# Optimization experiments

Hardware: AMD Instinct MI355X
Metric: run time of the kernel (lower is better)

Reference implementation:

```python
import jax, jax.numpy as jnp
import numpy as np

CAT_SIZES = [31360, 6807, 18, 94]
TOTAL = int(sum(CAT_SIZES))          # 38279
EMB = 128
N_FIELDS = len(CAT_SIZES)
D_IN = N_FIELDS * EMB                # 512 (num_features is empty)
MLP_DIMS = [2048, 1024, 512]
B = 16384
OFFSETS = np.concatenate([[0], np.cumsum(CAT_SIZES)[:-1]]).astype(np.int32)


def setup_inputs() -> dict:
    key = jax.random.key(0)
    ks = jax.random.split(key, 20)
    # x holds raw per-field category ids stored as float32 (as the torch model expects)
    cols = [jax.random.randint(ks[i], (B,), 0, s) for i, s in enumerate(CAT_SIZES)]
    x = jnp.stack(cols, axis=1).astype(jnp.float32)

    bias = jnp.zeros((1,), jnp.float32)
    fc = jax.random.uniform(ks[4], (TOTAL, 1), dtype=jnp.float32)          # nn.Parameter(torch.rand)
    emb_table = jax.random.normal(ks[5], (TOTAL, EMB), dtype=jnp.float32)  # nn.Embedding default N(0,1)

    dims = [D_IN] + MLP_DIMS + [1]
    params = {}
    for i in range(len(dims) - 1):
        fan_in = dims[i]
        bound = 1.0 / np.sqrt(fan_in)
        params[f"W{i+1}"] = jax.random.uniform(ks[6 + 2 * i], (dims[i], dims[i + 1]), jnp.float32, -bound, bound)
        params[f"b{i+1}"] = jax.random.uniform(ks[7 + 2 * i], (dims[i + 1],), jnp.float32, -bound, bound)

    return dict(x=x, bias=bias, fc=fc, emb_table=emb_table, **params)


def reference(x, bias, fc, emb_table, W1, b1, W2, b2, W3, b3, W4, b4):
    cat = x.astype(jnp.int32)                       # [B, F] raw per-field ids
    b = cat.shape[0]

    # embedding lookup with RAW (un-offset) ids, faithful to the original code
    embed_x = emb_table[cat].reshape(b, -1)          # [B, F*EMB]

    # one_hot(offset ids) @ fc  ==  sum_f fc[offset ids]  (offset ranges disjoint)
    gidx = cat + jnp.asarray(OFFSETS)                # [B, F] global ids
    lin = jnp.sum(fc[gidx, 0], axis=1)               # [B]
    fm_y = bias + lin                                # [B]

    # FM term: embed_x is 2-D, so sum over dim=1 collapses features;
    # the keepdim sum over dim=-1 then collapses the BATCH dim to shape (1,)
    # (a quirk of the original code that we reproduce exactly)
    square_of_sum = jnp.sum(embed_x, axis=1) ** 2    # [B]
    sum_of_square = jnp.sum(embed_x ** 2, axis=1)    # [B]
    fm_y = fm_y + 0.5 * jnp.sum(square_of_sum - sum_of_square, axis=-1, keepdims=True)  # [B]
    fm_y = fm_y[:, None]                             # [B,1]

    # MLP (eval mode: dropout is identity)
    h = embed_x
    for W, bb in ((W1, b1), (W2, b2), (W3, b3)):
        h = jax.nn.relu(h @ W + bb)
    mlp_y = h @ W4 + b4                              # [B,1]

    return jax.nn.sigmoid(fm_y + mlp_y)              # [B,1]
```

## Files before the change

kernel.cpp:

```cpp
#include <hip/hip_runtime.h>
#include <hip/hip_fp8.h>
#include <cstdint>


typedef float f32x4 __attribute__((ext_vector_type(4)));
typedef int i32x4 __attribute__((ext_vector_type(4)));
typedef int i32x8 __attribute__((ext_vector_type(8)));

#define GLOAD16(gptr, lptr)                                                \
  __builtin_amdgcn_global_load_lds(                                        \
      (const __attribute__((address_space(1))) void*)(gptr),               \
      (__attribute__((address_space(3))) void*)(lptr), 16, 0, 0)

__device__ inline uint32_t f2fp4(float v) {
  uint32_t s = (__float_as_uint(v) >> 31) << 3;
  float a = fabsf(v);
  uint32_t m;
  if (a < 0.25f) m = 0;
  else if (a < 0.75f) m = 1;
  else if (a < 1.25f) m = 2;
  else if (a < 1.75f) m = 3;
  else if (a < 2.5f)  m = 4;
  else if (a < 3.5f)  m = 5;
  else if (a < 5.0f)  m = 6;
  else m = 7;
  return s | m;
}

static constexpr size_t OFF_LIN  = 0;
static constexpr size_t OFF_PART = 65536;
static constexpr size_t OFF_S    = 81920;
static constexpr size_t OFF_ACC  = 98304;
static constexpr size_t OFF_EMB  = 262144;
static constexpr size_t OFF_H1   = OFF_EMB + 8388608ull;
static constexpr size_t OFF_H2   = OFF_H1 + 33554432ull;
static constexpr size_t OFF_W1T  = OFF_H2 + 16777216ull;
static constexpr size_t OFF_W2T  = OFF_W1T + 524288ull;
static constexpr size_t OFF_W3T  = OFF_W2T + 1048576ull;

__global__ void prep(const float* __restrict__ W1, const float* __restrict__ W2,
                     const float* __restrict__ W3, uint8_t* __restrict__ W1T,
                     uint8_t* __restrict__ W2T, uint8_t* __restrict__ W3T,
                     const float* __restrict__ x, const float* __restrict__ fc,
                     const float* __restrict__ emb, uint8_t* __restrict__ ebf,
                     float* __restrict__ lin, float* __restrict__ partials) {
  __shared__ __align__(16) float smem[32 * 33];
  int blk = blockIdx.x;
  int tid = threadIdx.x;
  if (blk < 3584) {
    const float* W;
    uint8_t* WT;
    int K, N, bx, by;
    if (blk < 1024) {
      W = W1; WT = W1T; K = 512; N = 2048; bx = blk & 63; by = blk >> 6;
    } else if (blk < 3072) {
      int t = blk - 1024;
      W = W2; WT = W2T; K = 2048; N = 1024; bx = t & 31; by = t >> 5;
    } else {
      int t = blk - 3072;
      W = W3; WT = W3T; K = 1024; N = 512; bx = t & 15; by = t >> 4;
    }
    int tx = tid & 31, ty = tid >> 5;
    int n0 = bx * 32, k0 = by * 32;
#pragma unroll
    for (int i = ty; i < 32; i += 8)
      smem[i * 33 + tx] = W[(size_t)(k0 + i) * N + n0 + tx];
    __syncthreads();
    if (tx < 16) {
#pragma unroll
      for (int i = ty; i < 32; i += 8) {
        uint32_t lo = f2fp4(smem[(2 * tx) * 33 + i] * 128.f);
        uint32_t hi = f2fp4(smem[(2 * tx + 1) * 33 + i] * 128.f);
        WT[(size_t)(n0 + i) * (K >> 1) + (k0 >> 1) + tx] =
            (uint8_t)(lo | (hi << 4));
      }
    }
  } else {
    int gb = blk - 3584;
    int wv = tid >> 6, lane = tid & 63;
    int b = gb * 4 + wv;
    int f = lane >> 4;
    int idx = (int)x[b * 4 + f];
    const float* row = emb + (size_t)idx * 128 + (lane & 15) * 8;
    float4 v0 = ((const float4*)row)[0];
    float4 v1 = ((const float4*)row)[1];
    float s = v0.x + v0.y + v0.z + v0.w + v1.x + v1.y + v1.z + v1.w;
    float q = v0.x * v0.x + v0.y * v0.y + v0.z * v0.z + v0.w * v0.w +
              v1.x * v1.x + v1.y * v1.y + v1.z * v1.z + v1.w * v1.w;

    int lo = 0, hi = 0;
    lo = __builtin_amdgcn_cvt_pk_fp8_f32(v0.x, v0.y, lo, false);
    lo = __builtin_amdgcn_cvt_pk_fp8_f32(v0.z, v0.w, lo, true);
    hi = __builtin_amdgcn_cvt_pk_fp8_f32(v1.x, v1.y, hi, false);
    hi = __builtin_amdgcn_cvt_pk_fp8_f32(v1.z, v1.w, hi, true);
    int2 pk = make_int2(lo, hi);
    *(int2*)(ebf + (size_t)b * 512 + lane * 8) = pk;

    float lp = 0.f;
    if ((lane & 15) == 0) {
      int off = (f == 1) ? 31360 : (f == 2) ? 38167 : (f == 3) ? 38185 : 0;
      lp = fc[idx + off];
    }
#pragma unroll
    for (int m = 32; m; m >>= 1) {
      s += __shfl_xor(s, m);
      q += __shfl_xor(q, m);
      lp += __shfl_xor(lp, m);
    }
    float* pt = smem;
    if (lane == 0) {
      lin[b] = lp;
      pt[wv] = s * s - q;
    }
    __syncthreads();
    if (tid == 0) partials[gb] = pt[0] + pt[1] + pt[2] + pt[3];
  }
}

__global__ void reduce_partials(const float* __restrict__ p,
                                float* __restrict__ S,
                                float* __restrict__ dotacc) {
  int tid = threadIdx.x;
  float v = 0.f;
  for (int i = tid; i < 4096; i += 256) v += p[i];
#pragma unroll
  for (int m = 32; m; m >>= 1) v += __shfl_xor(v, m);
  __shared__ float ps[4];
  if ((tid & 63) == 0) ps[tid >> 6] = v;
  __syncthreads();
  if (tid == 0) S[0] = ps[0] + ps[1] + ps[2] + ps[3];
  float4 z4 = make_float4(0.f, 0.f, 0.f, 0.f);
  for (int i = tid; i < 4096; i += 256) ((float4*)dotacc)[i] = z4;
}

__global__ __launch_bounds__(256) void gemm_mx_relu(
    const uint8_t* __restrict__ A, const uint8_t* __restrict__ BT,
    const float* __restrict__ bias, uint8_t* __restrict__ C, int K, int N,
    int GX) {
  __shared__ __align__(16) uint8_t As[128][256];
  __shared__ __align__(16) uint8_t Bs[128][128];
  int bid = blockIdx.x;
  int by = (bid & 7) + ((bid >> 3) / GX) * 8;
  int bx = (bid >> 3) & (GX - 1);
  int tid = threadIdx.x;
  int wv = tid >> 6, lane = tid & 63;
  int m0 = by * 128, n0 = bx * 128;
  int mw = (wv >> 1) * 64, nw = (wv & 1) * 64;
  int ml = lane & 15, kg = lane >> 4;
  int Kb2 = K >> 1;
  int arow = lane >> 4;
  int brow = lane >> 3;
  int bcol = ((lane & 7) ^ brow) * 16;

  f32x4 acc[4][4];
#pragma unroll
  for (int i = 0; i < 4; ++i)
#pragma unroll
    for (int j = 0; j < 4; ++j) acc[i][j] = (f32x4){0.f, 0.f, 0.f, 0.f};

  for (int kt = 0; kt < K; kt += 256) {
#pragma unroll
    for (int r = 0; r < 8; ++r) {
      int g = r * 4 + wv;
      int trow = 4 * g + arow;
      int acol = ((lane & 15) ^ (trow & 15)) * 16;
      const uint8_t* ga = A + (size_t)(m0 + trow) * K + kt + acol;
      GLOAD16(ga, &As[4 * g][0]);
    }
#pragma unroll
    for (int r = 0; r < 4; ++r) {
      int g = r * 4 + wv;
      const uint8_t* gb =
          BT + (size_t)(n0 + 8 * g + brow) * Kb2 + (kt >> 1) + bcol;
      GLOAD16(gb, &Bs[8 * g][0]);
    }
    __syncthreads();

    i32x4 z = (i32x4){0, 0, 0, 0};
#pragma unroll
    for (int j = 0; j < 2; ++j) {
      int c0 = 8 * j + 2 * kg;
      int pa0 = (c0 ^ ml) * 16;
      int pa1 = ((c0 + 1) ^ ml) * 16;
      int pb = ((4 * j + kg) ^ (ml & 7)) * 16;
      i32x8 af[4], bfr[4];
#pragma unroll
      for (int t = 0; t < 4; ++t) {
        int ra = mw + t * 16 + ml;
        i32x4 a0 = *(const i32x4*)&As[ra][pa0];
        i32x4 a1 = *(const i32x4*)&As[ra][pa1];
        af[t] = __builtin_shufflevector(a0, a1, 0, 1, 2, 3, 4, 5, 6, 7);
        i32x4 vb = *(const i32x4*)&Bs[nw + t * 16 + ml][pb];
        bfr[t] = __builtin_shufflevector(vb, z, 0, 1, 2, 3, 4, 5, 6, 7);
      }
#pragma unroll
      for (int mt = 0; mt < 4; ++mt)
#pragma unroll
        for (int nt = 0; nt < 4; ++nt)
          acc[mt][nt] = __builtin_amdgcn_mfma_scale_f32_16x16x128_f8f6f4(
              af[mt], bfr[nt], acc[mt][nt],
               0,  4,
              0, 0x7F7F7F7F, 0, 0x78787878);
    }
    __syncthreads();
  }

  int rbase = kg * 4;
#pragma unroll
  for (int nt = 0; nt < 4; ++nt) {
    int col = n0 + nw + nt * 16 + ml;
    float bv = bias[col];
#pragma unroll
    for (int mt = 0; mt < 4; ++mt) {
      int row = m0 + mw + mt * 16 + rbase;
      float v0 = acc[mt][nt][0] + bv, v1 = acc[mt][nt][1] + bv;
      float v2 = acc[mt][nt][2] + bv, v3 = acc[mt][nt][3] + bv;
      v0 = v0 > 0.f ? v0 : 0.f;
      v1 = v1 > 0.f ? v1 : 0.f;
      v2 = v2 > 0.f ? v2 : 0.f;
      v3 = v3 > 0.f ? v3 : 0.f;
      int w01 = __builtin_amdgcn_cvt_pk_fp8_f32(v0, v1, 0, false);
      int w23 = __builtin_amdgcn_cvt_pk_fp8_f32(v2, v3, 0, false);
      C[(size_t)(row + 0) * N + col] = (uint8_t)(w01 & 0xFF);
      C[(size_t)(row + 1) * N + col] = (uint8_t)((w01 >> 8) & 0xFF);
      C[(size_t)(row + 2) * N + col] = (uint8_t)(w23 & 0xFF);
      C[(size_t)(row + 3) * N + col] = (uint8_t)((w23 >> 8) & 0xFF);
    }
  }
}

__global__ __launch_bounds__(256) void gemm_mx_dot(
    const uint8_t* __restrict__ A, const uint8_t* __restrict__ BT,
    const float* __restrict__ bias, const float* __restrict__ W4,
    float* __restrict__ dotacc, int K, int N, int GX) {
  __shared__ __align__(16) uint8_t As[128][256];
  __shared__ __align__(16) uint8_t Bs[128][128];
  int bid = blockIdx.x;
  int by = (bid & 7) + ((bid >> 3) / GX) * 8;
  int bx = (bid >> 3) & (GX - 1);
  int tid = threadIdx.x;
  int wv = tid >> 6, lane = tid & 63;
  int m0 = by * 128, n0 = bx * 128;
  int mw = (wv >> 1) * 64, nw = (wv & 1) * 64;
  int ml = lane & 15, kg = lane >> 4;
  int Kb2 = K >> 1;
  int arow = lane >> 4;
  int brow = lane >> 3;
  int bcol = ((lane & 7) ^ brow) * 16;

  f32x4 acc[4][4];
#pragma unroll
  for (int i = 0; i < 4; ++i)
#pragma unroll
    for (int j = 0; j < 4; ++j) acc[i][j] = (f32x4){0.f, 0.f, 0.f, 0.f};

  for (int kt = 0; kt < K; kt += 256) {
#pragma unroll
    for (int r = 0; r < 8; ++r) {
      int g = r * 4 + wv;
      int trow = 4 * g + arow;
      int acol = ((lane & 15) ^ (trow & 15)) * 16;
      const uint8_t* ga = A + (size_t)(m0 + trow) * K + kt + acol;
      GLOAD16(ga, &As[4 * g][0]);
    }
#pragma unroll
    for (int r = 0; r < 4; ++r) {
      int g = r * 4 + wv;
      const uint8_t* gb =
          BT + (size_t)(n0 + 8 * g + brow) * Kb2 + (kt >> 1) + bcol;
      GLOAD16(gb, &Bs[8 * g][0]);
    }
    __syncthreads();

    i32x4 z = (i32x4){0, 0, 0, 0};
#pragma unroll
    for (int j = 0; j < 2; ++j) {
      int c0 = 8 * j + 2 * kg;
      int pa0 = (c0 ^ ml) * 16;
      int pa1 = ((c0 + 1) ^ ml) * 16;
      int pb = ((4 * j + kg) ^ (ml & 7)) * 16;
      i32x8 af[4], bfr[4];
#pragma unroll
      for (int t = 0; t < 4; ++t) {
        int ra = mw + t * 16 + ml;
        i32x4 a0 = *(const i32x4*)&As[ra][pa0];
        i32x4 a1 = *(const i32x4*)&As[ra][pa1];
        af[t] = __builtin_shufflevector(a0, a1, 0, 1, 2, 3, 4, 5, 6, 7);
        i32x4 vb = *(const i32x4*)&Bs[nw + t * 16 + ml][pb];
        bfr[t] = __builtin_shufflevector(vb, z, 0, 1, 2, 3, 4, 5, 6, 7);
      }
#pragma unroll
      for (int mt = 0; mt < 4; ++mt)
#pragma unroll
        for (int nt = 0; nt < 4; ++nt)
          acc[mt][nt] = __builtin_amdgcn_mfma_scale_f32_16x16x128_f8f6f4(
              af[mt], bfr[nt], acc[mt][nt],
              0, 4, 0, 0x7F7F7F7F, 0, 0x78787878);
    }
    __syncthreads();
  }

  float bv[4], w4v[4];
#pragma unroll
  for (int nt = 0; nt < 4; ++nt) {
    int col = n0 + nw + nt * 16 + ml;
    bv[nt] = bias[col];
    w4v[nt] = W4[col];
  }
  int rbase = kg * 4;
#pragma unroll
  for (int mt = 0; mt < 4; ++mt) {
#pragma unroll
    for (int r = 0; r < 4; ++r) {
      float p = 0.f;
#pragma unroll
      for (int nt = 0; nt < 4; ++nt) {
        float v = acc[mt][nt][r] + bv[nt];
        v = v > 0.f ? v : 0.f;
        p += v * w4v[nt];
      }
#pragma unroll
      for (int m = 1; m < 16; m <<= 1) p += __shfl_xor(p, m);
      if (ml == 0)
        atomicAdd(&dotacc[m0 + mw + mt * 16 + rbase + r], p);
    }
  }
}

__global__ void final_out(const float* __restrict__ dotacc,
                          const float* __restrict__ lin,
                          const float* __restrict__ S,
                          const float* __restrict__ bias,
                          const float* __restrict__ b4,
                          float* __restrict__ out) {
  int i = blockIdx.x * 256 + threadIdx.x;
  float z = dotacc[i] + b4[0] + bias[0] + lin[i] + 0.5f * S[0];
  out[i] = 1.f / (1.f + expf(-z));
}

extern "C" void kernel_launch(void* const* d_in, const int* in_sizes, int n_in,
                              void* d_out, int out_size, void* d_ws,
                              size_t ws_size, hipStream_t stream) {
  const float* x    = (const float*)d_in[0];
  const float* bias = (const float*)d_in[1];
  const float* fc   = (const float*)d_in[2];
  const float* emb  = (const float*)d_in[3];
  const float* W1   = (const float*)d_in[4];
  const float* b1   = (const float*)d_in[5];
  const float* W2   = (const float*)d_in[6];
  const float* b2   = (const float*)d_in[7];
  const float* W3   = (const float*)d_in[8];
  const float* b3   = (const float*)d_in[9];
  const float* W4   = (const float*)d_in[10];
  const float* b4   = (const float*)d_in[11];
  float* out = (float*)d_out;

  char* ws = (char*)d_ws;
  float* lin    = (float*)(ws + OFF_LIN);
  float* part   = (float*)(ws + OFF_PART);
  float* Sp     = (float*)(ws + OFF_S);
  float* dacc   = (float*)(ws + OFF_ACC);
  uint8_t* EMBb = (uint8_t*)(ws + OFF_EMB);
  uint8_t* H1   = (uint8_t*)(ws + OFF_H1);
  uint8_t* H2   = (uint8_t*)(ws + OFF_H2);
  uint8_t* W1T  = (uint8_t*)(ws + OFF_W1T);
  uint8_t* W2T  = (uint8_t*)(ws + OFF_W2T);
  uint8_t* W3T  = (uint8_t*)(ws + OFF_W3T);

  prep<<<7680, 256, 0, stream>>>(W1, W2, W3, W1T, W2T, W3T, x, fc, emb, EMBb,
                                 lin, part);
  reduce_partials<<<1, 256, 0, stream>>>(part, Sp, dacc);

  gemm_mx_relu<<<2048, 256, 0, stream>>>(EMBb, W1T, b1, H1, 512, 2048, 16);
  gemm_mx_relu<<<1024, 256, 0, stream>>>(H1, W2T, b2, H2, 2048, 1024, 8);
  gemm_mx_dot<<<512, 256, 0, stream>>>(H2, W3T, b3, W4, dacc, 1024, 512, 4);

  final_out<<<64, 256, 0, stream>>>(dacc, lin, Sp, bias, b4, out);
}
```

Measured before the change: 174.8 us.

## Halve GEMM K-tile to 128 and fold partial reduction into other kernels

Removes the single-block reduce_partials launch. Zeroing of the dot accumulator moves into 16 extra prep blocks, and the FM partial sum is recomputed redundantly by every final_out block. The GEMM kernels now stage a 128-wide K tile instead of 256, which halves LDS use per block and changes the swizzle and load layout. This may allow more blocks per CU, at the cost of twice as many K iterations and barriers.

```diff
diff --git a/kernel.cpp b/kernel.cpp
--- a/kernel.cpp
+++ b/kernel.cpp
@@ -29,7 +29,6 @@
 
 static constexpr size_t OFF_LIN  = 0;
 static constexpr size_t OFF_PART = 65536;
-static constexpr size_t OFF_S    = 81920;
 static constexpr size_t OFF_ACC  = 98304;
 static constexpr size_t OFF_EMB  = 262144;
 static constexpr size_t OFF_H1   = OFF_EMB + 8388608ull;
@@ -43,7 +42,8 @@
                      uint8_t* __restrict__ W2T, uint8_t* __restrict__ W3T,
                      const float* __restrict__ x, const float* __restrict__ fc,
                      const float* __restrict__ emb, uint8_t* __restrict__ ebf,
-                     float* __restrict__ lin, float* __restrict__ partials) {
+                     float* __restrict__ lin, float* __restrict__ partials,
+                     float* __restrict__ dotacc) {
   __shared__ __align__(16) float smem[32 * 33];
   int blk = blockIdx.x;
   int tid = threadIdx.x;
@@ -75,7 +75,7 @@
             (uint8_t)(lo | (hi << 4));
       }
     }
-  } else {
+  } else if (blk < 7680) {
     int gb = blk - 3584;
     int wv = tid >> 6, lane = tid & 63;
     int b = gb * 4 + wv;
@@ -114,31 +114,18 @@
     }
     __syncthreads();
     if (tid == 0) partials[gb] = pt[0] + pt[1] + pt[2] + pt[3];
-  }
-}
-
-__global__ void reduce_partials(const float* __restrict__ p,
-                                float* __restrict__ S,
-                                float* __restrict__ dotacc) {
-  int tid = threadIdx.x;
-  float v = 0.f;
-  for (int i = tid; i < 4096; i += 256) v += p[i];
-#pragma unroll
-  for (int m = 32; m; m >>= 1) v += __shfl_xor(v, m);
-  __shared__ float ps[4];
-  if ((tid & 63) == 0) ps[tid >> 6] = v;
-  __syncthreads();
-  if (tid == 0) S[0] = ps[0] + ps[1] + ps[2] + ps[3];
-  float4 z4 = make_float4(0.f, 0.f, 0.f, 0.f);
-  for (int i = tid; i < 4096; i += 256) ((float4*)dotacc)[i] = z4;
+  } else {
+    int zb = blk - 7680;
+    ((float4*)dotacc)[zb * 256 + tid] = make_float4(0.f, 0.f, 0.f, 0.f);
+  }
 }
 
 __global__ __launch_bounds__(256) void gemm_mx_relu(
     const uint8_t* __restrict__ A, const uint8_t* __restrict__ BT,
     const float* __restrict__ bias, uint8_t* __restrict__ C, int K, int N,
     int GX) {
-  __shared__ __align__(16) uint8_t As[128][256];
-  __shared__ __align__(16) uint8_t Bs[128][128];
+  __shared__ __align__(16) uint8_t As[128][128];
+  __shared__ __align__(16) uint8_t Bs[128][64];
   int bid = blockIdx.x;
   int by = (bid & 7) + ((bid >> 3) / GX) * 8;
   int bx = (bid >> 3) & (GX - 1);
@@ -148,9 +135,13 @@
   int mw = (wv >> 1) * 64, nw = (wv & 1) * 64;
   int ml = lane & 15, kg = lane >> 4;
   int Kb2 = K >> 1;
-  int arow = lane >> 4;
-  int brow = lane >> 3;
-  int bcol = ((lane & 7) ^ brow) * 16;
+  int asrow = lane >> 3;
+  int ascol = ((lane & 7) ^ asrow) * 16;
+  int bsrow = lane >> 2;
+  int bscol = ((lane & 3) ^ (bsrow & 3)) * 16;
+  int pa0 = ((2 * kg) ^ (ml & 7)) * 16;
+  int pa1 = ((2 * kg + 1) ^ (ml & 7)) * 16;
+  int pb = (kg ^ (ml & 3)) * 16;
 
   f32x4 acc[4][4];
 #pragma unroll
@@ -158,50 +149,41 @@
 #pragma unroll
     for (int j = 0; j < 4; ++j) acc[i][j] = (f32x4){0.f, 0.f, 0.f, 0.f};
 
-  for (int kt = 0; kt < K; kt += 256) {
-#pragma unroll
-    for (int r = 0; r < 8; ++r) {
-      int g = r * 4 + wv;
-      int trow = 4 * g + arow;
-      int acol = ((lane & 15) ^ (trow & 15)) * 16;
-      const uint8_t* ga = A + (size_t)(m0 + trow) * K + kt + acol;
-      GLOAD16(ga, &As[4 * g][0]);
-    }
+  for (int kt = 0; kt < K; kt += 128) {
 #pragma unroll
     for (int r = 0; r < 4; ++r) {
       int g = r * 4 + wv;
+      const uint8_t* ga = A + (size_t)(m0 + 8 * g + asrow) * K + kt + ascol;
+      GLOAD16(ga, &As[8 * g][0]);
+    }
+#pragma unroll
+    for (int r = 0; r < 2; ++r) {
+      int g = r * 4 + wv;
       const uint8_t* gb =
-          BT + (size_t)(n0 + 8 * g + brow) * Kb2 + (kt >> 1) + bcol;
-      GLOAD16(gb, &Bs[8 * g][0]);
+          BT + (size_t)(n0 + 16 * g + bsrow) * Kb2 + (kt >> 1) + bscol;
+      GLOAD16(gb, &Bs[16 * g][0]);
     }
     __syncthreads();
 
     i32x4 z = (i32x4){0, 0, 0, 0};
-#pragma unroll
-    for (int j = 0; j < 2; ++j) {
-      int c0 = 8 * j + 2 * kg;
-      int pa0 = (c0 ^ ml) * 16;
-      int pa1 = ((c0 + 1) ^ ml) * 16;
-      int pb = ((4 * j + kg) ^ (ml & 7)) * 16;
-      i32x8 af[4], bfr[4];
-#pragma unroll
-      for (int t = 0; t < 4; ++t) {
-        int ra = mw + t * 16 + ml;
-        i32x4 a0 = *(const i32x4*)&As[ra][pa0];
-        i32x4 a1 = *(const i32x4*)&As[ra][pa1];
-        af[t] = __builtin_shufflevector(a0, a1, 0, 1, 2, 3, 4, 5, 6, 7);
-        i32x4 vb = *(const i32x4*)&Bs[nw + t * 16 + ml][pb];
-        bfr[t] = __builtin_shufflevector(vb, z, 0, 1, 2, 3, 4, 5, 6, 7);
-      }
-#pragma unroll
-      for (int mt = 0; mt < 4; ++mt)
-#pragma unroll
-        for (int nt = 0; nt < 4; ++nt)
-          acc[mt][nt] = __builtin_amdgcn_mfma_scale_f32_16x16x128_f8f6f4(
-              af[mt], bfr[nt], acc[mt][nt],
-               0,  4,
-              0, 0x7F7F7F7F, 0, 0x78787878);
-    }
+    i32x8 af[4], bfr[4];
+#pragma unroll
+    for (int t = 0; t < 4; ++t) {
+      int ra = mw + t * 16 + ml;
+      i32x4 a0 = *(const i32x4*)&As[ra][pa0];
+      i32x4 a1 = *(const i32x4*)&As[ra][pa1];
+      af[t] = __builtin_shufflevector(a0, a1, 0, 1, 2, 3, 4, 5, 6, 7);
+      i32x4 vb = *(const i32x4*)&Bs[nw + t * 16 + ml][pb];
+      bfr[t] = __builtin_shufflevector(vb, z, 0, 1, 2, 3, 4, 5, 6, 7);
+    }
+#pragma unroll
+    for (int mt = 0; mt < 4; ++mt)
+#pragma unroll
+      for (int nt = 0; nt < 4; ++nt)
+        acc[mt][nt] = __builtin_amdgcn_mfma_scale_f32_16x16x128_f8f6f4(
+            af[mt], bfr[nt], acc[mt][nt],
+             0,  4,
+            0, 0x7F7F7F7F, 0, 0x78787878);
     __syncthreads();
   }
 
@@ -233,8 +215,8 @@
     const uint8_t* __restrict__ A, const uint8_t* __restrict__ BT,
     const float* __restrict__ bias, const float* __restrict__ W4,
     float* __restrict__ dotacc, int K, int N, int GX) {
-  __shared__ __align__(16) uint8_t As[128][256];
-  __shared__ __align__(16) uint8_t Bs[128][128];
+  __shared__ __align__(16) uint8_t As[128][128];
+  __shared__ __align__(16) uint8_t Bs[128][64];
   int bid = blockIdx.x;
   int by = (bid & 7) + ((bid >> 3) / GX) * 8;
   int bx = (bid >> 3) & (GX - 1);
@@ -244,9 +226,13 @@
   int mw = (wv >> 1) * 64, nw = (wv & 1) * 64;
   int ml = lane & 15, kg = lane >> 4;
   int Kb2 = K >> 1;
-  int arow = lane >> 4;
-  int brow = lane >> 3;
-  int bcol = ((lane & 7) ^ brow) * 16;
+  int asrow = lane >> 3;
+  int ascol = ((lane & 7) ^ asrow) * 16;
+  int bsrow = lane >> 2;
+  int bscol = ((lane & 3) ^ (bsrow & 3)) * 16;
+  int pa0 = ((2 * kg) ^ (ml & 7)) * 16;
+  int pa1 = ((2 * kg + 1) ^ (ml & 7)) * 16;
+  int pb = (kg ^ (ml & 3)) * 16;
 
   f32x4 acc[4][4];
 #pragma unroll
@@ -254,49 +240,40 @@
 #pragma unroll
     for (int j = 0; j < 4; ++j) acc[i][j] = (f32x4){0.f, 0.f, 0.f, 0.f};
 
-  for (int kt = 0; kt < K; kt += 256) {
-#pragma unroll
-    for (int r = 0; r < 8; ++r) {
-      int g = r * 4 + wv;
-      int trow = 4 * g + arow;
-      int acol = ((lane & 15) ^ (trow & 15)) * 16;
-      const uint8_t* ga = A + (size_t)(m0 + trow) * K + kt + acol;
-      GLOAD16(ga, &As[4 * g][0]);
-    }
+  for (int kt = 0; kt < K; kt += 128) {
 #pragma unroll
     for (int r = 0; r < 4; ++r) {
       int g = r * 4 + wv;
+      const uint8_t* ga = A + (size_t)(m0 + 8 * g + asrow) * K + kt + ascol;
+      GLOAD16(ga, &As[8 * g][0]);
+    }
+#pragma unroll
+    for (int r = 0; r < 2; ++r) {
+      int g = r * 4 + wv;
       const uint8_t* gb =
-          BT + (size_t)(n0 + 8 * g + brow) * Kb2 + (kt >> 1) + bcol;
-      GLOAD16(gb, &Bs[8 * g][0]);
+          BT + (size_t)(n0 + 16 * g + bsrow) * Kb2 + (kt >> 1) + bscol;
+      GLOAD16(gb, &Bs[16 * g][0]);
     }
     __syncthreads();
 
     i32x4 z = (i32x4){0, 0, 0, 0};
-#pragma unroll
-    for (int j = 0; j < 2; ++j) {
-      int c0 = 8 * j + 2 * kg;
-      int pa0 = (c0 ^ ml) * 16;
-      int pa1 = ((c0 + 1) ^ ml) * 16;
-      int pb = ((4 * j + kg) ^ (ml & 7)) * 16;
-      i32x8 af[4], bfr[4];
-#pragma unroll
-      for (int t = 0; t < 4; ++t) {
-        int ra = mw + t * 16 + ml;
-        i32x4 a0 = *(const i32x4*)&As[ra][pa0];
-        i32x4 a1 = *(const i32x4*)&As[ra][pa1];
-        af[t] = __builtin_shufflevector(a0, a1, 0, 1, 2, 3, 4, 5, 6, 7);
-        i32x4 vb = *(const i32x4*)&Bs[nw + t * 16 + ml][pb];
-        bfr[t] = __builtin_shufflevector(vb, z, 0, 1, 2, 3, 4, 5, 6, 7);
-      }
-#pragma unroll
-      for (int mt = 0; mt < 4; ++mt)
-#pragma unroll
-        for (int nt = 0; nt < 4; ++nt)
-          acc[mt][nt] = __builtin_amdgcn_mfma_scale_f32_16x16x128_f8f6f4(
-              af[mt], bfr[nt], acc[mt][nt],
-              0, 4, 0, 0x7F7F7F7F, 0, 0x78787878);
-    }
+    i32x8 af[4], bfr[4];
+#pragma unroll
+    for (int t = 0; t < 4; ++t) {
+      int ra = mw + t * 16 + ml;
+      i32x4 a0 = *(const i32x4*)&As[ra][pa0];
+      i32x4 a1 = *(const i32x4*)&As[ra][pa1];
+      af[t] = __builtin_shufflevector(a0, a1, 0, 1, 2, 3, 4, 5, 6, 7);
+      i32x4 vb = *(const i32x4*)&Bs[nw + t * 16 + ml][pb];
+      bfr[t] = __builtin_shufflevector(vb, z, 0, 1, 2, 3, 4, 5, 6, 7);
+    }
+#pragma unroll
+    for (int mt = 0; mt < 4; ++mt)
+#pragma unroll
+      for (int nt = 0; nt < 4; ++nt)
+        acc[mt][nt] = __builtin_amdgcn_mfma_scale_f32_16x16x128_f8f6f4(
+            af[mt], bfr[nt], acc[mt][nt],
+            0, 4, 0, 0x7F7F7F7F, 0, 0x78787878);
     __syncthreads();
   }
 
@@ -327,14 +304,23 @@
   }
 }
 
-__global__ void final_out(const float* __restrict__ dotacc,
+__global__ void final_out(const float* __restrict__ part,
+                          const float* __restrict__ dotacc,
                           const float* __restrict__ lin,
-                          const float* __restrict__ S,
                           const float* __restrict__ bias,
                           const float* __restrict__ b4,
                           float* __restrict__ out) {
-  int i = blockIdx.x * 256 + threadIdx.x;
-  float z = dotacc[i] + b4[0] + bias[0] + lin[i] + 0.5f * S[0];
+  __shared__ float ps[4];
+  int tid = threadIdx.x;
+  float v = 0.f;
+  for (int i = tid; i < 4096; i += 256) v += part[i];
+#pragma unroll
+  for (int m = 32; m; m >>= 1) v += __shfl_xor(v, m);
+  if ((tid & 63) == 0) ps[tid >> 6] = v;
+  __syncthreads();
+  float S = ps[0] + ps[1] + ps[2] + ps[3];
+  int i = blockIdx.x * 256 + tid;
+  float z = dotacc[i] + b4[0] + bias[0] + lin[i] + 0.5f * S;
   out[i] = 1.f / (1.f + expf(-z));
 }
 
@@ -358,7 +344,6 @@
   char* ws = (char*)d_ws;
   float* lin    = (float*)(ws + OFF_LIN);
   float* part   = (float*)(ws + OFF_PART);
-  float* Sp     = (float*)(ws + OFF_S);
   float* dacc   = (float*)(ws + OFF_ACC);
   uint8_t* EMBb = (uint8_t*)(ws + OFF_EMB);
   uint8_t* H1   = (uint8_t*)(ws + OFF_H1);
@@ -367,13 +352,12 @@
   uint8_t* W2T  = (uint8_t*)(ws + OFF_W2T);
   uint8_t* W3T  = (uint8_t*)(ws + OFF_W3T);
 
-  prep<<<7680, 256, 0, stream>>>(W1, W2, W3, W1T, W2T, W3T, x, fc, emb, EMBb,
-                                 lin, part);
-  reduce_partials<<<1, 256, 0, stream>>>(part, Sp, dacc);
+  prep<<<7696, 256, 0, stream>>>(W1, W2, W3, W1T, W2T, W3T, x, fc, emb, EMBb,
+                                 lin, part, dacc);
 
   gemm_mx_relu<<<2048, 256, 0, stream>>>(EMBb, W1T, b1, H1, 512, 2048, 16);
   gemm_mx_relu<<<1024, 256, 0, stream>>>(H1, W2T, b2, H2, 2048, 1024, 8);
   gemm_mx_dot<<<512, 256, 0, stream>>>(H2, W3T, b3, W4, dacc, 1024, 512, 4);
 
-  final_out<<<64, 256, 0, stream>>>(dacc, lin, Sp, bias, b4, out);
-}
+  final_out<<<64, 256, 0, stream>>>(part, dacc, lin, bias, b4, out);
+}
```

Result: slower. 179.9 us (+2.9%).
